# Performance work log

Measured on AMD Instinct MI355X. Metric: run time of the kernel, lower is better.

## Reference

```python
import jax, jax.numpy as jnp
import numpy as np

EMBED_DIM = 1024
HEADS = 16
HEAD_DIM = EMBED_DIM // HEADS


def setup_inputs() -> dict:
    key = jax.random.key(0)
    k1, k2, k3, k4 = jax.random.split(key, 4)
    x = jax.random.normal(k1, (4, 2048, EMBED_DIM), dtype=jnp.float32)
    # nn.Linear weights stored as (out, in); apply as x @ W.T
    W_qkv = jax.random.normal(k2, (3 * EMBED_DIM, EMBED_DIM), dtype=jnp.float32) / np.sqrt(EMBED_DIM)
    W_out = jax.random.normal(k3, (EMBED_DIM, EMBED_DIM), dtype=jnp.float32) / np.sqrt(EMBED_DIM)
    b_out = jax.random.normal(k4, (EMBED_DIM,), dtype=jnp.float32) * 0.02
    return {"x": x, "W_qkv": W_qkv, "W_out": W_out, "b_out": b_out}


def reference(x, W_qkv, W_out, b_out):
    B, N, _ = x.shape
    qkv = jnp.einsum('bnd,ed->bne', x, W_qkv)  # (B, N, 3*E)
    q, k, v = jnp.split(qkv, 3, axis=-1)
    # (B, H, N, Dh)
    q = q.reshape(B, N, HEADS, HEAD_DIM).transpose(0, 2, 1, 3)
    k = k.reshape(B, N, HEADS, HEAD_DIM).transpose(0, 2, 1, 3)
    v = v.reshape(B, N, HEADS, HEAD_DIM).transpose(0, 2, 1, 3)
    scale = 1.0 / np.sqrt(HEAD_DIM).astype(np.float32)
    scores = jnp.einsum('bhqd,bhkd->bhqk', q, k) * scale  # (B, H, N, N)
    attn = jax.nn.softmax(scores, axis=-1)
    out = jnp.einsum('bhqk,bhkd->bhqd', attn, v)  # (B, H, N, Dh)
    out = out.transpose(0, 2, 1, 3).reshape(B, N, EMBED_DIM)
    return jnp.einsum('bne,oe->bno', out, W_out) + b_out
```

## Files before the change

kernel.cpp:

```cpp
#include <hip/hip_runtime.h>
#include <hip/hip_bf16.h>
#include <stdint.h>


typedef _Float16 half8 __attribute__((ext_vector_type(8)));
typedef __fp16 fp16x2 __attribute__((ext_vector_type(2)));
typedef float floatx4 __attribute__((ext_vector_type(4)));

#define E 1024
#define NH 16
#define DH 64
#define SEQ 2048
#define BATCH 4

__device__ __forceinline__ void gload_lds16(const void* g, void* lds) {
  typedef __attribute__((address_space(1))) void gv;
  typedef __attribute__((address_space(3))) void lv;
  __builtin_amdgcn_global_load_lds((gv*)g, (lv*)lds, 16, 0, 0);
}

__device__ __forceinline__ float fast_exp2(float x) {
#if __has_builtin(__builtin_amdgcn_exp2f)
  return __builtin_amdgcn_exp2f(x);
#else
  return exp2f(x);
#endif
}

__global__ __launch_bounds__(256) void cvt_f32_f16(const float* __restrict__ in,
                                                   _Float16* __restrict__ out, int n8) {
  int i = blockIdx.x * 256 + threadIdx.x;
  if (i >= n8) return;
  const float4* p = (const float4*)in;
  float4 a = p[2 * i], b = p[2 * i + 1];
  half8 h;
  h[0] = (_Float16)a.x; h[1] = (_Float16)a.y; h[2] = (_Float16)a.z; h[3] = (_Float16)a.w;
  h[4] = (_Float16)b.x; h[5] = (_Float16)b.y; h[6] = (_Float16)b.z; h[7] = (_Float16)b.w;
  ((half8*)out)[i] = h;
}

__global__ __launch_bounds__(256)
void gemm_qkv(const _Float16* __restrict__ A, const _Float16* __restrict__ W,
              _Float16* __restrict__ qo, _Float16* __restrict__ ko, _Float16* __restrict__ vo) {
  __shared__ __align__(16) _Float16 As[128 * 64];
  __shared__ __align__(16) _Float16 Bs[128 * 64];
  const int t = threadIdx.x;
  const int w = t >> 6, l = t & 63;
  const int wr = w >> 1, wc = w & 1;
  const int lr = l & 15, hi = l >> 4;
  const int tileRow = blockIdx.y * 128;
  const int tileCol = blockIdx.x * 128;
  const int ldsW = (t & ~63) * 16;
  floatx4 acc[4][4] = {};

  for (int k0 = 0; k0 < 1024; k0 += 64) {
    __syncthreads();
#pragma unroll
    for (int c = 0; c < 4; ++c) {
      int idx = c * 256 + t;
      int row = idx >> 3, g = idx & 7;
      gload_lds16(A + (size_t)(tileRow + row) * 1024 + k0 + g * 8, (char*)As + c * 4096 + ldsW);
      gload_lds16(W + (size_t)(tileCol + row) * 1024 + k0 + g * 8, (char*)Bs + c * 4096 + ldsW);
    }
    __syncthreads();
#pragma unroll
    for (int kk = 0; kk < 2; ++kk) {
      half8 af[4], bf[4];
#pragma unroll
      for (int m = 0; m < 4; ++m)
        af[m] = *(const half8*)(As + (wr * 64 + m * 16 + lr) * 64 + kk * 32 + hi * 8);
#pragma unroll
      for (int n = 0; n < 4; ++n)
        bf[n] = *(const half8*)(Bs + (wc * 64 + n * 16 + lr) * 64 + kk * 32 + hi * 8);
#pragma unroll
      for (int m = 0; m < 4; ++m)
#pragma unroll
        for (int n = 0; n < 4; ++n)
          acc[m][n] = __builtin_amdgcn_mfma_f32_16x16x32_f16(af[m], bf[n], acc[m][n], 0, 0, 0);
    }
  }
  const int sec = tileCol >> 10;
  _Float16* dst = sec == 0 ? qo : (sec == 1 ? ko : vo);
  const float scaleq = sec == 0 ? 0.18033688011112042f : 1.0f;
  const int b = tileRow >> 11;
  const int tokBase = (tileRow & 2047) + wr * 64;
#pragma unroll
  for (int n = 0; n < 4; ++n) {
    int col = (tileCol & 1023) + wc * 64 + n * 16 + lr;
    int h = col >> 6, d = col & 63;
    _Float16* base = dst + (((size_t)b * NH + h) * SEQ + tokBase) * DH + d;
#pragma unroll
    for (int m = 0; m < 4; ++m)
#pragma unroll
      for (int j = 0; j < 4; ++j)
        base[(size_t)(m * 16 + hi * 4 + j) * DH] = (_Float16)(acc[m][n][j] * scaleq);
  }
}

__global__ __launch_bounds__(256)
void transpose_v(const _Float16* __restrict__ V, _Float16* __restrict__ VT) {
  __shared__ __align__(16) _Float16 L[64][80];
  const int bh = blockIdx.y, tt = blockIdx.x;
  const int t = threadIdx.x;
  const _Float16* vb = V + ((size_t)bh * SEQ + tt * 64) * DH;
#pragma unroll
  for (int c = 0; c < 2; ++c) {
    int idx = c * 256 + t;
    int row = idx >> 3, d0 = (idx & 7) * 8;
    *(half8*)&L[row][d0] = *(const half8*)(vb + row * DH + d0);
  }
  __syncthreads();
  _Float16* ob = VT + (size_t)bh * DH * SEQ + tt * 64;
#pragma unroll
  for (int c = 0; c < 2; ++c) {
    int idx = c * 256 + t;
    int d = idx >> 3, k0 = (idx & 7) * 8;
    half8 x;
#pragma unroll
    for (int jj = 0; jj < 8; ++jj) x[jj] = L[k0 + jj][d];
    *(half8*)(ob + (size_t)d * SEQ + k0) = x;
  }
}

__global__ __launch_bounds__(256)
void attn(const _Float16* __restrict__ Q, const _Float16* __restrict__ Kg,
          const _Float16* __restrict__ VT, _Float16* __restrict__ O) {
  __shared__ __align__(16) _Float16 Ks[64 * 64];
  __shared__ __align__(16) _Float16 Vs[64 * 64];
  __shared__ __align__(16) _Float16 Ps[4][16 * 64];
  const int bh = blockIdx.y, qt = blockIdx.x;
  const int t = threadIdx.x, w = t >> 6, l = t & 63;
  const int lr = l & 15, hi = l >> 4;
  const int ldsW = (t & ~63) * 16;
  const _Float16* qb = Q + ((size_t)bh * SEQ + qt * 64 + w * 16) * DH;
  half8 qf[2];
  qf[0] = *(const half8*)(qb + lr * DH + hi * 8);
  qf[1] = *(const half8*)(qb + lr * DH + 32 + hi * 8);
  floatx4 o_acc[4] = {};
  float m_run = -1e30f, l_run = 0.f;
  const _Float16* kb = Kg + (size_t)bh * SEQ * DH;
  const _Float16* vb = VT + (size_t)bh * DH * SEQ;
  char* pw = (char*)&Ps[w][0];
  const int lrm = lr & 7;
  uint32_t wra[4], rda[2];
#pragma unroll
  for (int n = 0; n < 4; ++n)
    wra[n] = lr * 128 + ((((2 * n + (hi >> 1)) ^ lrm)) << 4) + (hi & 1) * 8;
#pragma unroll
  for (int kk = 0; kk < 2; ++kk)
    rda[kk] = lr * 128 + (((4 * kk + hi) ^ lrm) << 4);

  for (int kt = 0; kt < SEQ / 64; ++kt) {
    __syncthreads();
#pragma unroll
    for (int c = 0; c < 2; ++c) {
      int idx = c * 256 + t;
      int row = idx >> 3, g = idx & 7, gs = g ^ (row & 7);
      gload_lds16(kb + (size_t)(kt * 64 + row) * DH + gs * 8, (char*)Ks + c * 4096 + ldsW);
      gload_lds16(vb + (size_t)row * SEQ + kt * 64 + gs * 8, (char*)Vs + c * 4096 + ldsW);
    }
    __syncthreads();
    floatx4 s[4] = {};
#pragma unroll
    for (int kk = 0; kk < 2; ++kk) {
      int gl = kk * 4 + hi;
#pragma unroll
      for (int n = 0; n < 4; ++n) {
        int key = n * 16 + lr;
        half8 af = *(const half8*)((char*)Ks + key * 128 + ((gl ^ (key & 7)) << 4));
        s[n] = __builtin_amdgcn_mfma_f32_16x16x32_f16(af, qf[kk], s[n], 0, 0, 0);
      }
    }
    float m01 = fmaxf(fmaxf(s[0][0], s[0][1]), fmaxf(s[0][2], s[0][3]));
    float m23 = fmaxf(fmaxf(s[1][0], s[1][1]), fmaxf(s[1][2], s[1][3]));
    float m45 = fmaxf(fmaxf(s[2][0], s[2][1]), fmaxf(s[2][2], s[2][3]));
    float m67 = fmaxf(fmaxf(s[3][0], s[3][1]), fmaxf(s[3][2], s[3][3]));
    float mx = fmaxf(fmaxf(m01, m23), fmaxf(m45, m67));
    mx = fmaxf(mx, __shfl_xor(mx, 16));
    mx = fmaxf(mx, __shfl_xor(mx, 32));
    if (__any(mx > m_run + 10.f)) {
      float mn = fmaxf(m_run, mx);
      float fac = fast_exp2(m_run - mn);
      m_run = mn;
      l_run *= fac;
#pragma unroll
      for (int j = 0; j < 4; ++j) {
        float fj = __shfl(fac, hi * 4 + j);
#pragma unroll
        for (int n = 0; n < 4; ++n) o_acc[n][j] *= fj;
      }
    }
    fp16x2 pk[4][2];
    float rs = 0.f;
#pragma unroll
    for (int n = 0; n < 4; ++n) {
      float p0 = fast_exp2(s[n][0] - m_run);
      float p1 = fast_exp2(s[n][1] - m_run);
      float p2 = fast_exp2(s[n][2] - m_run);
      float p3 = fast_exp2(s[n][3] - m_run);
      pk[n][0] = __builtin_amdgcn_cvt_pkrtz(p0, p1);
      pk[n][1] = __builtin_amdgcn_cvt_pkrtz(p2, p3);
      rs += p0 + p1 + p2 + p3;
    }
    rs += __shfl_xor(rs, 16);
    rs += __shfl_xor(rs, 32);
    l_run += rs;
#pragma unroll
    for (int n = 0; n < 4; ++n) {
      uint2 v;
      v.x = __builtin_bit_cast(uint32_t, pk[n][0]);
      v.y = __builtin_bit_cast(uint32_t, pk[n][1]);
      *(uint2*)(pw + wra[n]) = v;
    }
    half8 pf[2];
    pf[0] = *(const half8*)(pw + rda[0]);
    pf[1] = *(const half8*)(pw + rda[1]);
#pragma unroll
    for (int kk = 0; kk < 2; ++kk) {
      int gl = kk * 4 + hi;
#pragma unroll
      for (int n = 0; n < 4; ++n) {
        int d = n * 16 + lr;
        half8 vf = *(const half8*)((char*)Vs + d * 128 + ((gl ^ (d & 7)) << 4));
        o_acc[n] = __builtin_amdgcn_mfma_f32_16x16x32_f16(pf[kk], vf, o_acc[n], 0, 0, 0);
      }
    }
  }
  const int b = bh >> 4, h = bh & 15;
#pragma unroll
  for (int j = 0; j < 4; ++j) {
    float lj = __shfl(l_run, hi * 4 + j);
    float inv = 1.f / lj;
    int tok = qt * 64 + w * 16 + hi * 4 + j;
    _Float16* ob = O + ((size_t)b * SEQ + tok) * E + h * DH;
#pragma unroll
    for (int n = 0; n < 4; ++n) ob[n * 16 + lr] = (_Float16)(o_acc[n][j] * inv);
  }
}

__global__ __launch_bounds__(256)
void gemm_out(const _Float16* __restrict__ A, const _Float16* __restrict__ W,
              const float* __restrict__ bias, float* __restrict__ out) {
  __shared__ __align__(16) _Float16 As[128 * 64];
  __shared__ __align__(16) _Float16 Bs[128 * 64];
  const int t = threadIdx.x;
  const int w = t >> 6, l = t & 63;
  const int wr = w >> 1, wc = w & 1;
  const int lr = l & 15, hi = l >> 4;
  const int tileRow = blockIdx.y * 128;
  const int tileCol = blockIdx.x * 128;
  const int ldsW = (t & ~63) * 16;
  floatx4 acc[4][4] = {};

  for (int k0 = 0; k0 < 1024; k0 += 64) {
    __syncthreads();
#pragma unroll
    for (int c = 0; c < 4; ++c) {
      int idx = c * 256 + t;
      int row = idx >> 3, g = idx & 7;
      gload_lds16(A + (size_t)(tileRow + row) * 1024 + k0 + g * 8, (char*)As + c * 4096 + ldsW);
      gload_lds16(W + (size_t)(tileCol + row) * 1024 + k0 + g * 8, (char*)Bs + c * 4096 + ldsW);
    }
    __syncthreads();
#pragma unroll
    for (int kk = 0; kk < 2; ++kk) {
      half8 af[4], bf[4];
#pragma unroll
      for (int m = 0; m < 4; ++m)
        af[m] = *(const half8*)(As + (wr * 64 + m * 16 + lr) * 64 + kk * 32 + hi * 8);
#pragma unroll
      for (int n = 0; n < 4; ++n)
        bf[n] = *(const half8*)(Bs + (wc * 64 + n * 16 + lr) * 64 + kk * 32 + hi * 8);
#pragma unroll
      for (int m = 0; m < 4; ++m)
#pragma unroll
        for (int n = 0; n < 4; ++n)
          acc[m][n] = __builtin_amdgcn_mfma_f32_16x16x32_f16(af[m], bf[n], acc[m][n], 0, 0, 0);
    }
  }
#pragma unroll
  for (int n = 0; n < 4; ++n) {
    int col = tileCol + wc * 64 + n * 16 + lr;
    float bv = bias[col];
#pragma unroll
    for (int m = 0; m < 4; ++m) {
      int row = tileRow + wr * 64 + m * 16 + hi * 4;
#pragma unroll
      for (int j = 0; j < 4; ++j)
        out[(size_t)(row + j) * E + col] = acc[m][n][j] + bv;
    }
  }
}

extern "C" void kernel_launch(void* const* d_in, const int* in_sizes, int n_in,
                              void* d_out, int out_size, void* d_ws, size_t ws_size,
                              hipStream_t stream) {
  const float* x = (const float*)d_in[0];
  const float* Wqkv = (const float*)d_in[1];
  const float* Wout = (const float*)d_in[2];
  const float* bout = (const float*)d_in[3];
  float* out = (float*)d_out;
  char* ws = (char*)d_ws;
  _Float16* x16 = (_Float16*)(ws);
  _Float16* q16 = (_Float16*)(ws + (16u << 20));
  _Float16* k16 = (_Float16*)(ws + (32u << 20));
  _Float16* v16 = (_Float16*)(ws + (48u << 20));
  _Float16* wq16 = (_Float16*)(ws + (64u << 20));
  _Float16* wo16 = (_Float16*)(ws + (70u << 20));
  _Float16* vt16 = x16;
  _Float16* ao16 = v16;

  int n8x = in_sizes[0] / 8, n8q = in_sizes[1] / 8, n8o = in_sizes[2] / 8;
  cvt_f32_f16<<<(n8x + 255) / 256, 256, 0, stream>>>(x, x16, n8x);
  cvt_f32_f16<<<(n8q + 255) / 256, 256, 0, stream>>>(Wqkv, wq16, n8q);
  cvt_f32_f16<<<(n8o + 255) / 256, 256, 0, stream>>>(Wout, wo16, n8o);
  gemm_qkv<<<dim3(24, 64), 256, 0, stream>>>(x16, wq16, q16, k16, v16);
  transpose_v<<<dim3(32, 64), 256, 0, stream>>>(v16, vt16);
  attn<<<dim3(32, 64), 256, 0, stream>>>(q16, k16, vt16, ao16);
  gemm_out<<<dim3(8, 64), 256, 0, stream>>>(ao16, wo16, bout, out);
}
```

Before: 260.2 us.

## Double-buffer attention K/V tiles, fold max into MFMA, merge conversion kernels

The attention loop now double-buffers the K and V tiles in LDS, issuing the next tile's global-to-LDS loads before the current compute. This drops one barrier per iteration and lets memory traffic overlap the MFMAs. The running max is folded into the score accumulator's initial value, so the common no-rescale path skips a per-element subtract. The row-sum shuffles are deferred to the end, s_setprio is raised around the MFMA blocks, and the three fp32-to-fp16 conversion launches are merged into one. The cost is twice the K/V LDS footprint, which may lower occupancy, and a shared-memory hazard risk because there is no wait between the async loads and the barrier.

```diff
diff --git a/kernel.cpp b/kernel.cpp
--- a/kernel.cpp
+++ b/kernel.cpp
@@ -27,16 +27,24 @@
 #endif
 }
 
-__global__ __launch_bounds__(256) void cvt_f32_f16(const float* __restrict__ in,
-                                                   _Float16* __restrict__ out, int n8) {
+__global__ __launch_bounds__(256)
+void cvt3_f32_f16(const float* __restrict__ a, _Float16* __restrict__ oa, int na,
+                  const float* __restrict__ b, _Float16* __restrict__ ob, int nb,
+                  const float* __restrict__ c, _Float16* __restrict__ oc, int nc) {
   int i = blockIdx.x * 256 + threadIdx.x;
-  if (i >= n8) return;
+  const float* in;
+  _Float16* out;
+  int idx;
+  if (i < na) { in = a; out = oa; idx = i; }
+  else if (i < na + nb) { in = b; out = ob; idx = i - na; }
+  else if (i < na + nb + nc) { in = c; out = oc; idx = i - na - nb; }
+  else return;
   const float4* p = (const float4*)in;
-  float4 a = p[2 * i], b = p[2 * i + 1];
+  float4 u = p[2 * idx], v = p[2 * idx + 1];
   half8 h;
-  h[0] = (_Float16)a.x; h[1] = (_Float16)a.y; h[2] = (_Float16)a.z; h[3] = (_Float16)a.w;
-  h[4] = (_Float16)b.x; h[5] = (_Float16)b.y; h[6] = (_Float16)b.z; h[7] = (_Float16)b.w;
-  ((half8*)out)[i] = h;
+  h[0] = (_Float16)u.x; h[1] = (_Float16)u.y; h[2] = (_Float16)u.z; h[3] = (_Float16)u.w;
+  h[4] = (_Float16)v.x; h[5] = (_Float16)v.y; h[6] = (_Float16)v.z; h[7] = (_Float16)v.w;
+  ((half8*)out)[idx] = h;
 }
 
 __global__ __launch_bounds__(256)
@@ -125,8 +133,8 @@
 __global__ __launch_bounds__(256)
 void attn(const _Float16* __restrict__ Q, const _Float16* __restrict__ Kg,
           const _Float16* __restrict__ VT, _Float16* __restrict__ O) {
-  __shared__ __align__(16) _Float16 Ks[64 * 64];
-  __shared__ __align__(16) _Float16 Vs[64 * 64];
+  __shared__ __align__(16) _Float16 Ks[2][64 * 64];
+  __shared__ __align__(16) _Float16 Vs[2][64 * 64];
   __shared__ __align__(16) _Float16 Ps[4][16 * 64];
   const int bh = blockIdx.y, qt = blockIdx.x;
   const int t = threadIdx.x, w = t >> 6, l = t & 63;
@@ -137,7 +145,7 @@
   qf[0] = *(const half8*)(qb + lr * DH + hi * 8);
   qf[1] = *(const half8*)(qb + lr * DH + 32 + hi * 8);
   floatx4 o_acc[4] = {};
-  float m_run = -1e30f, l_run = 0.f;
+  float m_run = 0.f, l_run = 0.f;
   const _Float16* kb = Kg + (size_t)bh * SEQ * DH;
   const _Float16* vb = VT + (size_t)bh * DH * SEQ;
   char* pw = (char*)&Ps[w][0];
@@ -150,27 +158,35 @@
   for (int kk = 0; kk < 2; ++kk)
     rda[kk] = lr * 128 + (((4 * kk + hi) ^ lrm) << 4);
 
-  for (int kt = 0; kt < SEQ / 64; ++kt) {
-    __syncthreads();
+  auto stage = [&](int kt, int b) {
 #pragma unroll
     for (int c = 0; c < 2; ++c) {
       int idx = c * 256 + t;
       int row = idx >> 3, g = idx & 7, gs = g ^ (row & 7);
-      gload_lds16(kb + (size_t)(kt * 64 + row) * DH + gs * 8, (char*)Ks + c * 4096 + ldsW);
-      gload_lds16(vb + (size_t)row * SEQ + kt * 64 + gs * 8, (char*)Vs + c * 4096 + ldsW);
-    }
-    __syncthreads();
-    floatx4 s[4] = {};
+      gload_lds16(kb + (size_t)(kt * 64 + row) * DH + gs * 8, (char*)Ks[b] + c * 4096 + ldsW);
+      gload_lds16(vb + (size_t)row * SEQ + kt * 64 + gs * 8, (char*)Vs[b] + c * 4096 + ldsW);
+    }
+  };
+
+  stage(0, 0);
+  __syncthreads();
+  int buf = 0;
+  for (int kt = 0; kt < SEQ / 64; ++kt) {
+    if (kt + 1 < SEQ / 64) stage(kt + 1, buf ^ 1);
+    floatx4 cb = {-m_run, -m_run, -m_run, -m_run};
+    floatx4 s[4] = {cb, cb, cb, cb};
+    __builtin_amdgcn_s_setprio(1);
 #pragma unroll
     for (int kk = 0; kk < 2; ++kk) {
       int gl = kk * 4 + hi;
 #pragma unroll
       for (int n = 0; n < 4; ++n) {
         int key = n * 16 + lr;
-        half8 af = *(const half8*)((char*)Ks + key * 128 + ((gl ^ (key & 7)) << 4));
+        half8 af = *(const half8*)((char*)Ks[buf] + key * 128 + ((gl ^ (key & 7)) << 4));
         s[n] = __builtin_amdgcn_mfma_f32_16x16x32_f16(af, qf[kk], s[n], 0, 0, 0);
       }
     }
+    __builtin_amdgcn_s_setprio(0);
     float m01 = fmaxf(fmaxf(s[0][0], s[0][1]), fmaxf(s[0][2], s[0][3]));
     float m23 = fmaxf(fmaxf(s[1][0], s[1][1]), fmaxf(s[1][2], s[1][3]));
     float m45 = fmaxf(fmaxf(s[2][0], s[2][1]), fmaxf(s[2][2], s[2][3]));
@@ -178,10 +194,12 @@
     float mx = fmaxf(fmaxf(m01, m23), fmaxf(m45, m67));
     mx = fmaxf(mx, __shfl_xor(mx, 16));
     mx = fmaxf(mx, __shfl_xor(mx, 32));
-    if (__any(mx > m_run + 10.f)) {
-      float mn = fmaxf(m_run, mx);
-      float fac = fast_exp2(m_run - mn);
-      m_run = mn;
+    fp16x2 pk[4][2];
+    float rs;
+    if (__builtin_expect(__any(mx > 10.f), 0)) {
+      float dm = fmaxf(mx, 0.f);
+      float fac = fast_exp2(-dm);
+      m_run += dm;
       l_run *= fac;
 #pragma unroll
       for (int j = 0; j < 4; ++j) {
@@ -189,21 +207,26 @@
 #pragma unroll
         for (int n = 0; n < 4; ++n) o_acc[n][j] *= fj;
       }
-    }
-    fp16x2 pk[4][2];
-    float rs = 0.f;
-#pragma unroll
-    for (int n = 0; n < 4; ++n) {
-      float p0 = fast_exp2(s[n][0] - m_run);
-      float p1 = fast_exp2(s[n][1] - m_run);
-      float p2 = fast_exp2(s[n][2] - m_run);
-      float p3 = fast_exp2(s[n][3] - m_run);
-      pk[n][0] = __builtin_amdgcn_cvt_pkrtz(p0, p1);
-      pk[n][1] = __builtin_amdgcn_cvt_pkrtz(p2, p3);
-      rs += p0 + p1 + p2 + p3;
-    }
-    rs += __shfl_xor(rs, 16);
-    rs += __shfl_xor(rs, 32);
+      rs = 0.f;
+#pragma unroll
+      for (int n = 0; n < 4; ++n) {
+        float p0 = fast_exp2(s[n][0] - dm), p1 = fast_exp2(s[n][1] - dm);
+        float p2 = fast_exp2(s[n][2] - dm), p3 = fast_exp2(s[n][3] - dm);
+        pk[n][0] = __builtin_amdgcn_cvt_pkrtz(p0, p1);
+        pk[n][1] = __builtin_amdgcn_cvt_pkrtz(p2, p3);
+        rs += p0 + p1 + p2 + p3;
+      }
+    } else {
+      rs = 0.f;
+#pragma unroll
+      for (int n = 0; n < 4; ++n) {
+        float p0 = fast_exp2(s[n][0]), p1 = fast_exp2(s[n][1]);
+        float p2 = fast_exp2(s[n][2]), p3 = fast_exp2(s[n][3]);
+        pk[n][0] = __builtin_amdgcn_cvt_pkrtz(p0, p1);
+        pk[n][1] = __builtin_amdgcn_cvt_pkrtz(p2, p3);
+        rs += p0 + p1 + p2 + p3;
+      }
+    }
     l_run += rs;
 #pragma unroll
     for (int n = 0; n < 4; ++n) {
@@ -215,17 +238,23 @@
     half8 pf[2];
     pf[0] = *(const half8*)(pw + rda[0]);
     pf[1] = *(const half8*)(pw + rda[1]);
+    __builtin_amdgcn_s_setprio(1);
 #pragma unroll
     for (int kk = 0; kk < 2; ++kk) {
       int gl = kk * 4 + hi;
 #pragma unroll
       for (int n = 0; n < 4; ++n) {
         int d = n * 16 + lr;
-        half8 vf = *(const half8*)((char*)Vs + d * 128 + ((gl ^ (d & 7)) << 4));
+        half8 vf = *(const half8*)((char*)Vs[buf] + d * 128 + ((gl ^ (d & 7)) << 4));
         o_acc[n] = __builtin_amdgcn_mfma_f32_16x16x32_f16(pf[kk], vf, o_acc[n], 0, 0, 0);
       }
     }
-  }
+    __builtin_amdgcn_s_setprio(0);
+    __syncthreads();
+    buf ^= 1;
+  }
+  l_run += __shfl_xor(l_run, 16);
+  l_run += __shfl_xor(l_run, 32);
   const int b = bh >> 4, h = bh & 15;
 #pragma unroll
   for (int j = 0; j < 4; ++j) {
@@ -311,9 +340,8 @@
   _Float16* ao16 = v16;
 
   int n8x = in_sizes[0] / 8, n8q = in_sizes[1] / 8, n8o = in_sizes[2] / 8;
-  cvt_f32_f16<<<(n8x + 255) / 256, 256, 0, stream>>>(x, x16, n8x);
-  cvt_f32_f16<<<(n8q + 255) / 256, 256, 0, stream>>>(Wqkv, wq16, n8q);
-  cvt_f32_f16<<<(n8o + 255) / 256, 256, 0, stream>>>(Wout, wo16, n8o);
+  int n8 = n8x + n8q + n8o;
+  cvt3_f32_f16<<<(n8 + 255) / 256, 256, 0, stream>>>(x, x16, n8x, Wqkv, wq16, n8q, Wout, wo16, n8o);
   gemm_qkv<<<dim3(24, 64), 256, 0, stream>>>(x16, wq16, q16, k16, v16);
   transpose_v<<<dim3(32, 64), 256, 0, stream>>>(v16, vt16);
   attn<<<dim3(32, 64), 256, 0, stream>>>(q16, k16, vt16, ao16);
```

Measured after the change: 263.5 us. No clear change (+1.3%).
